# Kernel tuning notes

Measured on AMD Instinct MI355X. Metric: run time of the kernel, lower is better.

The kernel has to match this reference:

```python
import jax, jax.numpy as jnp
import numpy as np

N_NODES = 50000
N_EDGES = 800000
D_FEAT = 64
D_EMB = 64
N_GRAPHS = 512
D_TARGET = 10


def setup_inputs() -> dict:
    key = jax.random.key(0)
    ks = jax.random.split(key, 32)
    x = jax.random.normal(ks[0], (N_NODES, D_FEAT), dtype=jnp.float32)
    edge_index = jax.random.randint(ks[1], (2, N_EDGES), 0, N_NODES, dtype=jnp.int64)
    batch = jnp.sort(jax.random.randint(ks[2], (N_NODES,), 0, N_GRAPHS, dtype=jnp.int64))

    def lin(k, fan_in, fan_out):
        return jax.random.normal(k, (fan_in, fan_out), dtype=jnp.float32) / np.sqrt(fan_in)

    inp = {"x": x, "edge_index": edge_index, "batch": batch}
    # 3 SAGEConv layers: lin_l (neighbors, with bias) + lin_r (root, no bias)
    for i in range(3):
        din = D_FEAT if i == 0 else D_EMB
        inp[f"Wl{i}"] = lin(ks[3 + 3 * i], din, D_EMB)
        inp[f"bl{i}"] = jnp.zeros((D_EMB,), dtype=jnp.float32)
        inp[f"Wr{i}"] = lin(ks[4 + 3 * i], din, D_EMB)
    inp["Wm"] = lin(ks[20], D_EMB, D_EMB)
    inp["bm"] = jnp.zeros((D_EMB,), dtype=jnp.float32)
    inp["W1"] = lin(ks[21], 3 * D_EMB, D_EMB)
    inp["b1"] = jnp.zeros((D_EMB,), dtype=jnp.float32)
    inp["W2"] = lin(ks[22], D_EMB, D_TARGET)
    inp["b2"] = jnp.zeros((D_TARGET,), dtype=jnp.float32)
    return inp


def sage_conv(x, src, dst, Wl, bl, Wr):
    # mean-aggregate neighbor features (messages flow src -> dst)
    agg = jax.ops.segment_sum(x[src], dst, num_segments=N_NODES)
    deg = jax.ops.segment_sum(jnp.ones((src.shape[0],), x.dtype), dst, num_segments=N_NODES)
    mean = agg / jnp.maximum(deg, 1.0)[:, None]
    return mean @ Wl + bl + x @ Wr


def reference(x, edge_index, batch, Wl0, bl0, Wr0, Wl1, bl1, Wr1, Wl2, bl2, Wr2,
              Wm, bm, W1, b1, W2, b2):
    src, dst = edge_index[0], edge_index[1]
    convs = [(Wl0, bl0, Wr0), (Wl1, bl1, Wr1), (Wl2, bl2, Wr2)]
    h = x
    h_all = []
    for Wl, bl, Wr in convs:
        h = sage_conv(h, src, dst, Wl, bl, Wr)
        h = jax.nn.relu(h @ Wm + bm)
        h_all.append(h)
    h = jnp.concatenate(h_all, axis=1)  # [N, 3*D_EMB]
    # global mean pool over graphs
    gsum = jax.ops.segment_sum(h, batch, num_segments=N_GRAPHS)
    gcnt = jax.ops.segment_sum(jnp.ones((h.shape[0],), h.dtype), batch, num_segments=N_GRAPHS)
    g = gsum / jnp.maximum(gcnt, 1.0)[:, None]
    g = jax.nn.relu(g @ W1 + b1)
    return g @ W2 + b2
```

## Files before the change

kernel.cpp:

```cpp
#include <hip/hip_runtime.h>

#define N_NODES 50000
#define N_EDGES 800000
#define D 64
#define N_GRAPHS 512
#define D_TARGET 10
#define NB_SCAN ((N_NODES + 255) / 256)
#define TPAD 72
#define EDGE_BLOCKS (N_EDGES / 256)
#define XSPLIT_BLOCKS EDGE_BLOCKS
#define WPREP_BLOCKS 112

typedef __attribute__((ext_vector_type(8))) short short8;
typedef __attribute__((ext_vector_type(4))) float f32x4;
typedef unsigned short ushort_t;
#define MFMA16(a, b, c) __builtin_amdgcn_mfma_f32_16x16x32_bf16(a, b, c, 0, 0, 0)

__device__ inline unsigned short bf16rne(float f) {
    unsigned u = __builtin_bit_cast(unsigned, f);
    u += 0x7FFFu + ((u >> 16) & 1u);
    return (unsigned short)(u >> 16);
}
__device__ inline float bf2f(unsigned short h) {
    unsigned u = ((unsigned)h) << 16;
    return __builtin_bit_cast(float, u);
}
__device__ inline void acc8(float* a, uint4 v) {
    a[0] += __builtin_bit_cast(float, v.x << 16);
    a[1] += __builtin_bit_cast(float, v.x & 0xFFFF0000u);
    a[2] += __builtin_bit_cast(float, v.y << 16);
    a[3] += __builtin_bit_cast(float, v.y & 0xFFFF0000u);
    a[4] += __builtin_bit_cast(float, v.z << 16);
    a[5] += __builtin_bit_cast(float, v.z & 0xFFFF0000u);
    a[6] += __builtin_bit_cast(float, v.w << 16);
    a[7] += __builtin_bit_cast(float, v.w & 0xFFFF0000u);
}

__global__ void zero_kernel(int* __restrict__ degi) {
    int i = blockIdx.x * 256 + threadIdx.x;
    if (i < N_NODES) degi[i] = 0;
}

__global__ void k1_kernel(const int* __restrict__ dst, const int* __restrict__ batch,
                          int* __restrict__ degi, int* __restrict__ rank,
                          int* __restrict__ gstart,
                          const float* __restrict__ x, ushort_t* __restrict__ xh,
                          const float* __restrict__ w0, const float* __restrict__ w1,
                          const float* __restrict__ w2, const float* __restrict__ w3,
                          const float* __restrict__ w4, const float* __restrict__ w5,
                          const float* __restrict__ w6, short* __restrict__ wfrag) {
    int b = blockIdx.x;
    if (b < EDGE_BLOCKS) {
        int e = b * 256 + threadIdx.x;
        rank[e] = atomicAdd(&degi[dst[e]], 1);
    } else if (b < EDGE_BLOCKS + NB_SCAN) {
        int i = (b - EDGE_BLOCKS) * 256 + threadIdx.x;
        if (i >= N_NODES) return;
        int bb = batch[i];
        int prev = (i == 0) ? -1 : batch[i - 1];
        for (int g = prev + 1; g <= bb; ++g) gstart[g] = i;
        if (i == N_NODES - 1)
            for (int g = bb + 1; g <= N_GRAPHS; ++g) gstart[g] = N_NODES;
    } else if (b < EDGE_BLOCKS + NB_SCAN + XSPLIT_BLOCKS) {
        int idx = (b - EDGE_BLOCKS - NB_SCAN) * 256 + threadIdx.x;
        float4 v = ((const float4*)x)[idx];
        ushort4 o;
        o.x = bf16rne(v.x); o.y = bf16rne(v.y); o.z = bf16rne(v.z); o.w = bf16rne(v.w);
        ((ushort4*)xh)[idx] = o;
    } else {
        int tid = (b - EDGE_BLOCKS - NB_SCAN - XSPLIT_BLOCKS) * 256 + threadIdx.x;
        int m = tid >> 12, t = tid & 4095;
        const float* W = (m == 0) ? w0 : (m == 1) ? w1 : (m == 2) ? w2 : (m == 3) ? w3
                       : (m == 4) ? w4 : (m == 5) ? w5 : w6;
        int j = t & 7, lane = (t >> 3) & 63, nt = (t >> 9) & 3, kt = t >> 11;
        int k = kt * 32 + ((lane >> 4) << 3) + j;
        int o = nt * 16 + (lane & 15);
        float v = W[k * 64 + o];
        unsigned short hi = bf16rne(v);
        unsigned short lo = bf16rne(v - bf2f(hi));
        wfrag[m * 8192 + t]        = (short)hi;
        wfrag[m * 8192 + 4096 + t] = (short)lo;
    }
}

__global__ void scan_partials(const int* __restrict__ degi, int* __restrict__ partial) {
    __shared__ int s[256];
    int t = threadIdx.x;
    int i = blockIdx.x * 256 + t;
    s[t] = (i < N_NODES) ? degi[i] : 0;
    __syncthreads();
    for (int off = 128; off > 0; off >>= 1) {
        if (t < off) s[t] += s[t + off];
        __syncthreads();
    }
    if (t == 0) partial[blockIdx.x] = s[0];
}

__global__ void scan_final(const int* __restrict__ degi, const int* __restrict__ partial,
                           int* __restrict__ rowptr) {
    __shared__ int s[256];
    __shared__ int sp[256];
    int t = threadIdx.x;
    int i = blockIdx.x * 256 + t;
    sp[t] = (t < blockIdx.x) ? partial[t] : 0;
    __syncthreads();
    for (int off = 128; off > 0; off >>= 1) {
        if (t < off) sp[t] += sp[t + off];
        __syncthreads();
    }
    int prefix = sp[0];
    int v = (i < N_NODES) ? degi[i] : 0;
    s[t] = v;
    __syncthreads();
    for (int off = 1; off < 256; off <<= 1) {
        int add = (t >= off) ? s[t - off] : 0;
        __syncthreads();
        s[t] += add;
        __syncthreads();
    }
    if (i < N_NODES) rowptr[i] = prefix + s[t] - v;
    if (i == 0) rowptr[N_NODES] = N_EDGES;
}

__global__ void k4_kernel(const int* __restrict__ src, const int* __restrict__ dst,
                          const int* __restrict__ rank, const int* __restrict__ rowptr,
                          ushort_t* __restrict__ col) {
    int e = blockIdx.x * 256 + threadIdx.x;
    int d = dst[e];
    col[rowptr[d] + rank[e]] = (ushort_t)src[e];
}

__global__ __launch_bounds__(512) void gather_kernel(
    const ushort_t* __restrict__ hplane, const int* __restrict__ rowptr,
    const ushort_t* __restrict__ col,
    ushort_t* __restrict__ mh, ushort_t* __restrict__ ml) {
    int gw   = (blockIdx.x * 512 + threadIdx.x) >> 6;
    int lane = threadIdx.x & 63;
    int f = lane & 7;
    int g = lane >> 3;
    if (gw >= N_NODES) return;
    int beg = rowptr[gw], end = rowptr[gw + 1];
    const uint4* h16 = (const uint4*)hplane;

    float a[8] = {0.f, 0.f, 0.f, 0.f, 0.f, 0.f, 0.f, 0.f};
    float b[8] = {0.f, 0.f, 0.f, 0.f, 0.f, 0.f, 0.f, 0.f};
    int p = beg + g;
    for (; p + 8 < end; p += 16) {
        int s0 = col[p], s1 = col[p + 8];
        uint4 v0 = h16[s0 * 8 + f];
        uint4 v1 = h16[s1 * 8 + f];
        acc8(a, v0);
        acc8(b, v1);
    }
    if (p < end) {
        uint4 v = h16[col[p] * 8 + f];
        acc8(a, v);
    }
#pragma unroll
    for (int j = 0; j < 8; ++j) {
        float v = a[j] + b[j];
        v += __shfl_xor(v, 8);
        v += __shfl_xor(v, 16);
        v += __shfl_xor(v, 32);
        a[j] = v;
    }
    if (g == 0) {
        float inv = 1.0f / fmaxf((float)(end - beg), 1.0f);
        unsigned hws[4], lws[4];
#pragma unroll
        for (int i = 0; i < 4; ++i) {
            float v0 = a[2 * i] * inv, v1 = a[2 * i + 1] * inv;
            unsigned short h0 = bf16rne(v0), h1 = bf16rne(v1);
            hws[i] = (unsigned)h0 | ((unsigned)h1 << 16);
            lws[i] = (unsigned)bf16rne(v0 - bf2f(h0)) |
                     ((unsigned)bf16rne(v1 - bf2f(h1)) << 16);
        }
        uint4 hv = {hws[0], hws[1], hws[2], hws[3]};
        uint4 lv = {lws[0], lws[1], lws[2], lws[3]};
        ((uint4*)mh)[gw * 8 + f] = hv;
        ((uint4*)ml)[gw * 8 + f] = lv;
    }
}

template <int XMODE>
__global__ __launch_bounds__(64) void mm_kernel(
    const float* __restrict__ xf, const ushort_t* __restrict__ xhp,
    const ushort_t* __restrict__ mh, const ushort_t* __restrict__ ml,
    const short* __restrict__ wl, const short* __restrict__ wr, const short* __restrict__ wm,
    const float* __restrict__ blv, const float* __restrict__ bmv,
    ushort_t* __restrict__ hhout) {
    __shared__ short smh[16 * TPAD];
    __shared__ short sml[16 * TPAD];
    __shared__ short sxh[16 * TPAD];
    __shared__ short sxl[16 * TPAD];
    __shared__ short sth[16 * TPAD];
    __shared__ short stl[16 * TPAD];

    int lane = threadIdx.x;
    int f = lane & 15;
    int g = lane >> 4;
    int base = blockIdx.x * 16;

    {
        const uint4* mh16 = (const uint4*)mh;
        const uint4* ml16 = (const uint4*)ml;
#pragma unroll
        for (int i = 0; i < 2; ++i) {
            int c = i * 64 + lane;
            int r = c >> 3, cc = c & 7;
            *(uint4*)&smh[r * TPAD + cc * 8] = mh16[(base + r) * 8 + cc];
            *(uint4*)&sml[r * TPAD + cc * 8] = ml16[(base + r) * 8 + cc];
        }
    }
    if (XMODE == 1) {
        const uint4* xh16 = (const uint4*)xhp;
#pragma unroll
        for (int i = 0; i < 2; ++i) {
            int c = i * 64 + lane;
            int r = c >> 3, cc = c & 7;
            *(uint4*)&sxh[r * TPAD + cc * 8] = xh16[(base + r) * 8 + cc];
        }
    } else {
        const float4* x4 = (const float4*)xf;
#pragma unroll
        for (int i = 0; i < 4; ++i) {
            int idx = i * 64 + lane;
            int r = idx >> 4, c = idx & 15;
            float4 xv = x4[(size_t)(base + r) * 16 + c];
            unsigned short h0 = bf16rne(xv.x), h1 = bf16rne(xv.y),
                           h2 = bf16rne(xv.z), h3 = bf16rne(xv.w);
            uint2 hw, lw;
            hw.x = (unsigned)h0 | ((unsigned)h1 << 16);
            hw.y = (unsigned)h2 | ((unsigned)h3 << 16);
            lw.x = (unsigned)bf16rne(xv.x - bf2f(h0)) | ((unsigned)bf16rne(xv.y - bf2f(h1)) << 16);
            lw.y = (unsigned)bf16rne(xv.z - bf2f(h2)) | ((unsigned)bf16rne(xv.w - bf2f(h3)) << 16);
            *(uint2*)&sxh[r * TPAD + c * 4] = hw;
            *(uint2*)&sxl[r * TPAD + c * 4] = lw;
        }
    }

    short8 amh[2], aml[2], axh[2], axl[2];
#pragma unroll
    for (int kt = 0; kt < 2; ++kt) {
        int idx = f * TPAD + kt * 32 + g * 8;
        amh[kt] = *(const short8*)&smh[idx];
        aml[kt] = *(const short8*)&sml[idx];
        axh[kt] = *(const short8*)&sxh[idx];
        if (XMODE == 0) axl[kt] = *(const short8*)&sxl[idx];
    }
    const short* wlh = wl;
    const short* wll = wl + 4096;
    const short* wrh = wr;
    const short* wrl = wr + 4096;

#pragma unroll
    for (int nt = 0; nt < 4; ++nt) {
        f32x4 acc = {0.f, 0.f, 0.f, 0.f};
#pragma unroll
        for (int kt = 0; kt < 2; ++kt) {
            int fi = ((kt * 4 + nt) * 64 + lane) * 8;
            short8 blh = *(const short8*)&wlh[fi];
            short8 bll = *(const short8*)&wll[fi];
            short8 brh = *(const short8*)&wrh[fi];
            short8 brl = *(const short8*)&wrl[fi];
            acc = MFMA16(amh[kt], blh, acc);
            acc = MFMA16(aml[kt], blh, acc);
            acc = MFMA16(amh[kt], bll, acc);
            acc = MFMA16(axh[kt], brh, acc);
            if (XMODE == 0) acc = MFMA16(axl[kt], brh, acc);
            acc = MFMA16(axh[kt], brl, acc);
        }
        float bias = blv[nt * 16 + f];
#pragma unroll
        for (int r = 0; r < 4; ++r) {
            float tv = acc[r] + bias;
            unsigned short hi = bf16rne(tv);
            unsigned short lo = bf16rne(tv - bf2f(hi));
            int row = g * 4 + r;
            sth[row * TPAD + nt * 16 + f] = (short)hi;
            stl[row * TPAD + nt * 16 + f] = (short)lo;
        }
    }

    short8 ath[2], atl[2];
#pragma unroll
    for (int kt = 0; kt < 2; ++kt) {
        int idx = f * TPAD + kt * 32 + g * 8;
        ath[kt] = *(const short8*)&sth[idx];
        atl[kt] = *(const short8*)&stl[idx];
    }
    const short* wmh = wm;
    const short* wml = wm + 4096;
#pragma unroll
    for (int nt = 0; nt < 4; ++nt) {
        f32x4 acc = {0.f, 0.f, 0.f, 0.f};
#pragma unroll
        for (int kt = 0; kt < 2; ++kt) {
            int fi = ((kt * 4 + nt) * 64 + lane) * 8;
            short8 bh  = *(const short8*)&wmh[fi];
            short8 bl2 = *(const short8*)&wml[fi];
            acc = MFMA16(ath[kt], bh, acc);
            acc = MFMA16(atl[kt], bh, acc);
            acc = MFMA16(ath[kt], bl2, acc);
        }
        float bias = bmv[nt * 16 + f];
#pragma unroll
        for (int r = 0; r < 4; ++r) {
            float hv = acc[r] + bias;
            hv = hv > 0.f ? hv : 0.f;
            int row  = g * 4 + r;
            int node = base + row;
            hhout[node * D + nt * 16 + f] = bf16rne(hv);
        }
    }
}

__global__ __launch_bounds__(256) void poolmlp_kernel(
    const ushort_t* __restrict__ h0, const ushort_t* __restrict__ h1,
    const ushort_t* __restrict__ h2, const int* __restrict__ gstart,
    const float* __restrict__ W1, const float* __restrict__ b1,
    const float* __restrict__ W2, const float* __restrict__ b2,
    float* __restrict__ out) {
    __shared__ float spart[4][3][64];
    __shared__ float sg[3 * 64];
    __shared__ float tt[64];
    int gr = blockIdx.x;
    int w = threadIdx.x >> 6, lane = threadIdx.x & 63;
    int beg = gstart[gr], end = gstart[gr + 1];
    float s0 = 0.f, s1 = 0.f, s2 = 0.f;
    for (int n = beg + w; n < end; n += 4) {
        s0 += bf2f(h0[n * 64 + lane]);
        s1 += bf2f(h1[n * 64 + lane]);
        s2 += bf2f(h2[n * 64 + lane]);
    }
    spart[w][0][lane] = s0; spart[w][1][lane] = s1; spart[w][2][lane] = s2;
    __syncthreads();
    if (w == 0) {
        float inv = 1.0f / fmaxf((float)(end - beg), 1.0f);
#pragma unroll
        for (int l = 0; l < 3; ++l)
            sg[l * 64 + lane] = (spart[0][l][lane] + spart[1][l][lane] +
                                 spart[2][l][lane] + spart[3][l][lane]) * inv;
    }
    __syncthreads();
    if (w == 0) {
        float acc = b1[lane];
#pragma unroll 8
        for (int k = 0; k < 3 * 64; ++k) acc += sg[k] * W1[k * 64 + lane];
        tt[lane] = fmaxf(acc, 0.f);
    }
    __syncthreads();
    if (w == 0 && lane < D_TARGET) {
        float acc = b2[lane];
#pragma unroll
        for (int k = 0; k < 64; ++k) acc += tt[k] * W2[k * D_TARGET + lane];
        out[gr * D_TARGET + lane] = acc;
    }
}

extern "C" void kernel_launch(void* const* d_in, const int* in_sizes, int n_in,
                              void* d_out, int out_size, void* d_ws, size_t ws_size,
                              hipStream_t stream) {
    const float* x     = (const float*)d_in[0];
    const int*   ei    = (const int*)d_in[1];
    const int*   src   = ei;
    const int*   dst   = ei + N_EDGES;
    const int*   batch = (const int*)d_in[2];

    const float* Wl[3] = {(const float*)d_in[3], (const float*)d_in[6], (const float*)d_in[9]};
    const float* bl[3] = {(const float*)d_in[4], (const float*)d_in[7], (const float*)d_in[10]};
    const float* Wr[3] = {(const float*)d_in[5], (const float*)d_in[8], (const float*)d_in[11]};
    const float* Wm = (const float*)d_in[12];
    const float* bm = (const float*)d_in[13];
    const float* W1 = (const float*)d_in[14];
    const float* b1 = (const float*)d_in[15];
    const float* W2 = (const float*)d_in[16];
    const float* b2 = (const float*)d_in[17];

    int*      degi    = (int*)d_ws;
    int*      partial = degi + 50000;
    int*      rowptr  = partial + 256;
    int*      rank    = rowptr + 50008;
    int*      gstart  = rank + 800000;
    short*    wfrag   = (short*)(gstart + 520);
    ushort_t* col     = (ushort_t*)(wfrag + 7 * 8192);
    ushort_t* xh      = col + 800000;
    ushort_t* mh      = xh + (size_t)N_NODES * D;
    ushort_t* ml      = mh + (size_t)N_NODES * D;
    ushort_t* hh0     = ml + (size_t)N_NODES * D;
    ushort_t* hh1     = hh0 + (size_t)N_NODES * D;
    ushort_t* hh2     = hh1 + (size_t)N_NODES * D;

    zero_kernel<<<NB_SCAN, 256, 0, stream>>>(degi);

    k1_kernel<<<EDGE_BLOCKS + NB_SCAN + XSPLIT_BLOCKS + WPREP_BLOCKS, 256, 0, stream>>>(
        dst, batch, degi, rank, gstart, x, xh,
        Wl[0], Wr[0], Wl[1], Wr[1], Wl[2], Wr[2], Wm, wfrag);
    scan_partials<<<NB_SCAN, 256, 0, stream>>>(degi, partial);
    scan_final<<<NB_SCAN, 256, 0, stream>>>(degi, partial, rowptr);
    k4_kernel<<<EDGE_BLOCKS, 256, 0, stream>>>(src, dst, rank, rowptr, col);

    ushort_t* hplanes[4] = {xh, hh0, hh1, hh2};
    for (int l = 0; l < 3; ++l) {
        gather_kernel<<<(N_NODES * 64 + 511) / 512, 512, 0, stream>>>(
            hplanes[l], rowptr, col, mh, ml);
        if (l == 0)
            mm_kernel<0><<<N_NODES / 16, 64, 0, stream>>>(
                x, nullptr, mh, ml,
                wfrag + 0 * 8192, wfrag + 1 * 8192, wfrag + 6 * 8192,
                bl[0], bm, hh0);
        else
            mm_kernel<1><<<N_NODES / 16, 64, 0, stream>>>(
                nullptr, hplanes[l], mh, ml,
                wfrag + (2 * l) * 8192, wfrag + (2 * l + 1) * 8192, wfrag + 6 * 8192,
                bl[l], bm, hplanes[l + 1]);
    }

    poolmlp_kernel<<<N_GRAPHS, 256, 0, stream>>>(hh0, hh1, hh2, gstart, W1, b1, W2, b2,
                                                 (float*)d_out);
}
```

Before: 185.9 us.

## Split degree-count atomics across eight partitioned counter arrays

The per-destination degree counting in the CSR build now uses eight separate counter arrays, chosen by block index, so that contended atomics on the same node are spread out. A new combine kernel turns the per-partition counts into exclusive offsets and totals per node, and the column-scatter kernel adds the partition offset to each edge's local rank. The cost is an extra kernel launch, eight times more counters to zero and read, and an extra gather of the offset in the scatter step. Edge order within a node's row changes, so the floating-point sum order in the gather differs slightly.

After: 186.8 us. No clear change (+0.5%).

```diff
diff --git a/kernel.cpp b/kernel.cpp
--- a/kernel.cpp
+++ b/kernel.cpp
@@ -10,6 +10,8 @@
 #define EDGE_BLOCKS (N_EDGES / 256)
 #define XSPLIT_BLOCKS EDGE_BLOCKS
 #define WPREP_BLOCKS 112
+#define NPART 8
+#define PSTRIDE 50048
 
 typedef __attribute__((ext_vector_type(8))) short short8;
 typedef __attribute__((ext_vector_type(4))) float f32x4;
@@ -36,13 +38,13 @@
     a[7] += __builtin_bit_cast(float, v.w & 0xFFFF0000u);
 }
 
-__global__ void zero_kernel(int* __restrict__ degi) {
+__global__ void zero_kernel(int* __restrict__ deg8) {
     int i = blockIdx.x * 256 + threadIdx.x;
-    if (i < N_NODES) degi[i] = 0;
+    if (i < NPART * PSTRIDE) deg8[i] = 0;
 }
 
 __global__ void k1_kernel(const int* __restrict__ dst, const int* __restrict__ batch,
-                          int* __restrict__ degi, int* __restrict__ rank,
+                          int* __restrict__ deg8, int* __restrict__ rank,
                           int* __restrict__ gstart,
                           const float* __restrict__ x, ushort_t* __restrict__ xh,
                           const float* __restrict__ w0, const float* __restrict__ w1,
@@ -51,8 +53,10 @@
                           const float* __restrict__ w6, short* __restrict__ wfrag) {
     int b = blockIdx.x;
     if (b < EDGE_BLOCKS) {
+        int part = b & (NPART - 1);
         int e = b * 256 + threadIdx.x;
-        rank[e] = atomicAdd(&degi[dst[e]], 1);
+        int lr = atomicAdd(&deg8[part * PSTRIDE + dst[e]], 1);
+        rank[e] = (part << 24) | lr;
     } else if (b < EDGE_BLOCKS + NB_SCAN) {
         int i = (b - EDGE_BLOCKS) * 256 + threadIdx.x;
         if (i >= N_NODES) return;
@@ -83,6 +87,19 @@
     }
 }
 
+__global__ void combine_kernel(int* __restrict__ deg8, int* __restrict__ degi) {
+    int i = blockIdx.x * 256 + threadIdx.x;
+    if (i >= N_NODES) return;
+    int run = 0;
+#pragma unroll
+    for (int p = 0; p < NPART; ++p) {
+        int c = deg8[p * PSTRIDE + i];
+        deg8[p * PSTRIDE + i] = run;
+        run += c;
+    }
+    degi[i] = run;
+}
+
 __global__ void scan_partials(const int* __restrict__ degi, int* __restrict__ partial) {
     __shared__ int s[256];
     int t = threadIdx.x;
@@ -124,10 +141,13 @@
 
 __global__ void k4_kernel(const int* __restrict__ src, const int* __restrict__ dst,
                           const int* __restrict__ rank, const int* __restrict__ rowptr,
-                          ushort_t* __restrict__ col) {
+                          const int* __restrict__ deg8, ushort_t* __restrict__ col) {
     int e = blockIdx.x * 256 + threadIdx.x;
     int d = dst[e];
-    col[rowptr[d] + rank[e]] = (ushort_t)src[e];
+    int r = rank[e];
+    int part = r >> 24;
+    int pos = rowptr[d] + deg8[part * PSTRIDE + d] + (r & 0xFFFFFF);
+    col[pos] = (ushort_t)src[e];
 }
 
 __global__ __launch_bounds__(512) void gather_kernel(
@@ -377,7 +397,8 @@
     const float* W2 = (const float*)d_in[16];
     const float* b2 = (const float*)d_in[17];
 
-    int*      degi    = (int*)d_ws;
+    int*      deg8    = (int*)d_ws;
+    int*      degi    = deg8 + NPART * PSTRIDE;
     int*      partial = degi + 50000;
     int*      rowptr  = partial + 256;
     int*      rank    = rowptr + 50008;
@@ -391,14 +412,15 @@
     ushort_t* hh1     = hh0 + (size_t)N_NODES * D;
     ushort_t* hh2     = hh1 + (size_t)N_NODES * D;
 
-    zero_kernel<<<NB_SCAN, 256, 0, stream>>>(degi);
+    zero_kernel<<<(NPART * PSTRIDE + 255) / 256, 256, 0, stream>>>(deg8);
 
     k1_kernel<<<EDGE_BLOCKS + NB_SCAN + XSPLIT_BLOCKS + WPREP_BLOCKS, 256, 0, stream>>>(
-        dst, batch, degi, rank, gstart, x, xh,
+        dst, batch, deg8, rank, gstart, x, xh,
         Wl[0], Wr[0], Wl[1], Wr[1], Wl[2], Wr[2], Wm, wfrag);
+    combine_kernel<<<NB_SCAN, 256, 0, stream>>>(deg8, degi);
     scan_partials<<<NB_SCAN, 256, 0, stream>>>(degi, partial);
     scan_final<<<NB_SCAN, 256, 0, stream>>>(degi, partial, rowptr);
-    k4_kernel<<<EDGE_BLOCKS, 256, 0, stream>>>(src, dst, rank, rowptr, col);
+    k4_kernel<<<EDGE_BLOCKS, 256, 0, stream>>>(src, dst, rank, rowptr, deg8, col);
 
     ushort_t* hplanes[4] = {xh, hh0, hh1, hh2};
     for (int l = 0; l < 3; ++l) {
```

## Fuse neighbor gather with SAGE matmuls into one kernel per layer

Applied to the files above, without the earlier changes.

Merges the mean-aggregation gather kernel and the MFMA matmul kernel into a single 1024-thread block per 16 nodes. Each of the 16 waves gathers one node's neighbors into shared memory, then four waves run the Wl/Wr and Wm MFMA stages. This removes the global round-trip of the split-bf16 mean planes and half the kernel launches. In exchange, 12 of 16 waves sit idle during the matmul phase, and the large blocks may limit occupancy and tail behaviour.

Result: slower. 202.1 us (+8.7%).

```diff
diff --git a/kernel.cpp b/kernel.cpp
--- a/kernel.cpp
+++ b/kernel.cpp
@@ -130,62 +130,10 @@
     col[rowptr[d] + rank[e]] = (ushort_t)src[e];
 }
 
-__global__ __launch_bounds__(512) void gather_kernel(
-    const ushort_t* __restrict__ hplane, const int* __restrict__ rowptr,
-    const ushort_t* __restrict__ col,
-    ushort_t* __restrict__ mh, ushort_t* __restrict__ ml) {
-    int gw   = (blockIdx.x * 512 + threadIdx.x) >> 6;
-    int lane = threadIdx.x & 63;
-    int f = lane & 7;
-    int g = lane >> 3;
-    if (gw >= N_NODES) return;
-    int beg = rowptr[gw], end = rowptr[gw + 1];
-    const uint4* h16 = (const uint4*)hplane;
-
-    float a[8] = {0.f, 0.f, 0.f, 0.f, 0.f, 0.f, 0.f, 0.f};
-    float b[8] = {0.f, 0.f, 0.f, 0.f, 0.f, 0.f, 0.f, 0.f};
-    int p = beg + g;
-    for (; p + 8 < end; p += 16) {
-        int s0 = col[p], s1 = col[p + 8];
-        uint4 v0 = h16[s0 * 8 + f];
-        uint4 v1 = h16[s1 * 8 + f];
-        acc8(a, v0);
-        acc8(b, v1);
-    }
-    if (p < end) {
-        uint4 v = h16[col[p] * 8 + f];
-        acc8(a, v);
-    }
-#pragma unroll
-    for (int j = 0; j < 8; ++j) {
-        float v = a[j] + b[j];
-        v += __shfl_xor(v, 8);
-        v += __shfl_xor(v, 16);
-        v += __shfl_xor(v, 32);
-        a[j] = v;
-    }
-    if (g == 0) {
-        float inv = 1.0f / fmaxf((float)(end - beg), 1.0f);
-        unsigned hws[4], lws[4];
-#pragma unroll
-        for (int i = 0; i < 4; ++i) {
-            float v0 = a[2 * i] * inv, v1 = a[2 * i + 1] * inv;
-            unsigned short h0 = bf16rne(v0), h1 = bf16rne(v1);
-            hws[i] = (unsigned)h0 | ((unsigned)h1 << 16);
-            lws[i] = (unsigned)bf16rne(v0 - bf2f(h0)) |
-                     ((unsigned)bf16rne(v1 - bf2f(h1)) << 16);
-        }
-        uint4 hv = {hws[0], hws[1], hws[2], hws[3]};
-        uint4 lv = {lws[0], lws[1], lws[2], lws[3]};
-        ((uint4*)mh)[gw * 8 + f] = hv;
-        ((uint4*)ml)[gw * 8 + f] = lv;
-    }
-}
-
 template <int XMODE>
-__global__ __launch_bounds__(64) void mm_kernel(
-    const float* __restrict__ xf, const ushort_t* __restrict__ xhp,
-    const ushort_t* __restrict__ mh, const ushort_t* __restrict__ ml,
+__global__ __launch_bounds__(1024) void sage_fused(
+    const float* __restrict__ xf, const ushort_t* __restrict__ hplane,
+    const int* __restrict__ rowptr, const ushort_t* __restrict__ col,
     const short* __restrict__ wl, const short* __restrict__ wr, const short* __restrict__ wm,
     const float* __restrict__ blv, const float* __restrict__ bmv,
     ushort_t* __restrict__ hhout) {
@@ -196,65 +144,99 @@
     __shared__ short sth[16 * TPAD];
     __shared__ short stl[16 * TPAD];
 
-    int lane = threadIdx.x;
+    int tid  = threadIdx.x;
+    int wid  = tid >> 6;
+    int lane = tid & 63;
+    int f8 = lane & 7;
+    int g8 = lane >> 3;
+    int base = blockIdx.x * 16;
+    int node = base + wid;
+    const uint4* h16 = (const uint4*)hplane;
+
+    {
+        int beg = rowptr[node], end = rowptr[node + 1];
+        float a[8] = {0.f, 0.f, 0.f, 0.f, 0.f, 0.f, 0.f, 0.f};
+        float b[8] = {0.f, 0.f, 0.f, 0.f, 0.f, 0.f, 0.f, 0.f};
+        int p = beg + g8;
+        for (; p + 8 < end; p += 16) {
+            int s0 = col[p], s1 = col[p + 8];
+            uint4 v0 = h16[s0 * 8 + f8];
+            uint4 v1 = h16[s1 * 8 + f8];
+            acc8(a, v0);
+            acc8(b, v1);
+        }
+        if (p < end) {
+            uint4 v = h16[col[p] * 8 + f8];
+            acc8(a, v);
+        }
+#pragma unroll
+        for (int j = 0; j < 8; ++j) {
+            float v = a[j] + b[j];
+            v += __shfl_xor(v, 8);
+            v += __shfl_xor(v, 16);
+            v += __shfl_xor(v, 32);
+            a[j] = v;
+        }
+        if (g8 == 0) {
+            float inv = 1.0f / fmaxf((float)(end - beg), 1.0f);
+            unsigned hws[4], lws[4];
+#pragma unroll
+            for (int i = 0; i < 4; ++i) {
+                float v0 = a[2 * i] * inv, v1 = a[2 * i + 1] * inv;
+                unsigned short h0 = bf16rne(v0), h1 = bf16rne(v1);
+                hws[i] = (unsigned)h0 | ((unsigned)h1 << 16);
+                lws[i] = (unsigned)bf16rne(v0 - bf2f(h0)) |
+                         ((unsigned)bf16rne(v1 - bf2f(h1)) << 16);
+            }
+            uint4 hv = {hws[0], hws[1], hws[2], hws[3]};
+            uint4 lv = {lws[0], lws[1], lws[2], lws[3]};
+            *(uint4*)&smh[wid * TPAD + f8 * 8] = hv;
+            *(uint4*)&sml[wid * TPAD + f8 * 8] = lv;
+        } else if (g8 == 1) {
+            if (XMODE == 1) {
+                uint4 v = h16[node * 8 + f8];
+                *(uint4*)&sxh[wid * TPAD + f8 * 8] = v;
+            } else {
+                const float4* x4 = (const float4*)xf;
+                float4 v0 = x4[(size_t)node * 16 + f8 * 2];
+                float4 v1 = x4[(size_t)node * 16 + f8 * 2 + 1];
+                unsigned short h0 = bf16rne(v0.x), h1 = bf16rne(v0.y),
+                               h2 = bf16rne(v0.z), h3 = bf16rne(v0.w);
+                unsigned short h4 = bf16rne(v1.x), h5 = bf16rne(v1.y),
+                               h6 = bf16rne(v1.z), h7 = bf16rne(v1.w);
+                uint4 hv, lv;
+                hv.x = (unsigned)h0 | ((unsigned)h1 << 16);
+                hv.y = (unsigned)h2 | ((unsigned)h3 << 16);
+                hv.z = (unsigned)h4 | ((unsigned)h5 << 16);
+                hv.w = (unsigned)h6 | ((unsigned)h7 << 16);
+                lv.x = (unsigned)bf16rne(v0.x - bf2f(h0)) | ((unsigned)bf16rne(v0.y - bf2f(h1)) << 16);
+                lv.y = (unsigned)bf16rne(v0.z - bf2f(h2)) | ((unsigned)bf16rne(v0.w - bf2f(h3)) << 16);
+                lv.z = (unsigned)bf16rne(v1.x - bf2f(h4)) | ((unsigned)bf16rne(v1.y - bf2f(h5)) << 16);
+                lv.w = (unsigned)bf16rne(v1.z - bf2f(h6)) | ((unsigned)bf16rne(v1.w - bf2f(h7)) << 16);
+                *(uint4*)&sxh[wid * TPAD + f8 * 8] = hv;
+                *(uint4*)&sxl[wid * TPAD + f8 * 8] = lv;
+            }
+        }
+    }
+    __syncthreads();
+
     int f = lane & 15;
     int g = lane >> 4;
-    int base = blockIdx.x * 16;
-
-    {
-        const uint4* mh16 = (const uint4*)mh;
-        const uint4* ml16 = (const uint4*)ml;
-#pragma unroll
-        for (int i = 0; i < 2; ++i) {
-            int c = i * 64 + lane;
-            int r = c >> 3, cc = c & 7;
-            *(uint4*)&smh[r * TPAD + cc * 8] = mh16[(base + r) * 8 + cc];
-            *(uint4*)&sml[r * TPAD + cc * 8] = ml16[(base + r) * 8 + cc];
-        }
-    }
-    if (XMODE == 1) {
-        const uint4* xh16 = (const uint4*)xhp;
-#pragma unroll
-        for (int i = 0; i < 2; ++i) {
-            int c = i * 64 + lane;
-            int r = c >> 3, cc = c & 7;
-            *(uint4*)&sxh[r * TPAD + cc * 8] = xh16[(base + r) * 8 + cc];
-        }
-    } else {
-        const float4* x4 = (const float4*)xf;
-#pragma unroll
-        for (int i = 0; i < 4; ++i) {
-            int idx = i * 64 + lane;
-            int r = idx >> 4, c = idx & 15;
-            float4 xv = x4[(size_t)(base + r) * 16 + c];
-            unsigned short h0 = bf16rne(xv.x), h1 = bf16rne(xv.y),
-                           h2 = bf16rne(xv.z), h3 = bf16rne(xv.w);
-            uint2 hw, lw;
-            hw.x = (unsigned)h0 | ((unsigned)h1 << 16);
-            hw.y = (unsigned)h2 | ((unsigned)h3 << 16);
-            lw.x = (unsigned)bf16rne(xv.x - bf2f(h0)) | ((unsigned)bf16rne(xv.y - bf2f(h1)) << 16);
-            lw.y = (unsigned)bf16rne(xv.z - bf2f(h2)) | ((unsigned)bf16rne(xv.w - bf2f(h3)) << 16);
-            *(uint2*)&sxh[r * TPAD + c * 4] = hw;
-            *(uint2*)&sxl[r * TPAD + c * 4] = lw;
-        }
-    }
-
-    short8 amh[2], aml[2], axh[2], axl[2];
-#pragma unroll
-    for (int kt = 0; kt < 2; ++kt) {
-        int idx = f * TPAD + kt * 32 + g * 8;
-        amh[kt] = *(const short8*)&smh[idx];
-        aml[kt] = *(const short8*)&sml[idx];
-        axh[kt] = *(const short8*)&sxh[idx];
-        if (XMODE == 0) axl[kt] = *(const short8*)&sxl[idx];
-    }
-    const short* wlh = wl;
-    const short* wll = wl + 4096;
-    const short* wrh = wr;
-    const short* wrl = wr + 4096;
-
-#pragma unroll
-    for (int nt = 0; nt < 4; ++nt) {
+    if (wid < 4) {
+        int nt = wid;
+        short8 amh[2], aml[2], axh[2], axl[2];
+#pragma unroll
+        for (int kt = 0; kt < 2; ++kt) {
+            int idx = f * TPAD + kt * 32 + g * 8;
+            amh[kt] = *(const short8*)&smh[idx];
+            aml[kt] = *(const short8*)&sml[idx];
+            axh[kt] = *(const short8*)&sxh[idx];
+            if (XMODE == 0) axl[kt] = *(const short8*)&sxl[idx];
+        }
+        const short* wlh = wl;
+        const short* wll = wl + 4096;
+        const short* wrh = wr;
+        const short* wrl = wr + 4096;
         f32x4 acc = {0.f, 0.f, 0.f, 0.f};
 #pragma unroll
         for (int kt = 0; kt < 2; ++kt) {
@@ -281,18 +263,19 @@
             stl[row * TPAD + nt * 16 + f] = (short)lo;
         }
     }
-
-    short8 ath[2], atl[2];
-#pragma unroll
-    for (int kt = 0; kt < 2; ++kt) {
-        int idx = f * TPAD + kt * 32 + g * 8;
-        ath[kt] = *(const short8*)&sth[idx];
-        atl[kt] = *(const short8*)&stl[idx];
-    }
-    const short* wmh = wm;
-    const short* wml = wm + 4096;
-#pragma unroll
-    for (int nt = 0; nt < 4; ++nt) {
+    __syncthreads();
+
+    if (wid < 4) {
+        int nt = wid;
+        short8 ath[2], atl[2];
+#pragma unroll
+        for (int kt = 0; kt < 2; ++kt) {
+            int idx = f * TPAD + kt * 32 + g * 8;
+            ath[kt] = *(const short8*)&sth[idx];
+            atl[kt] = *(const short8*)&stl[idx];
+        }
+        const short* wmh = wm;
+        const short* wml = wm + 4096;
         f32x4 acc = {0.f, 0.f, 0.f, 0.f};
 #pragma unroll
         for (int kt = 0; kt < 2; ++kt) {
@@ -309,8 +292,8 @@
             float hv = acc[r] + bias;
             hv = hv > 0.f ? hv : 0.f;
             int row  = g * 4 + r;
-            int node = base + row;
-            hhout[node * D + nt * 16 + f] = bf16rne(hv);
+            int onode = base + row;
+            hhout[onode * D + nt * 16 + f] = bf16rne(hv);
         }
     }
 }
@@ -385,9 +368,7 @@
     short*    wfrag   = (short*)(gstart + 520);
     ushort_t* col     = (ushort_t*)(wfrag + 7 * 8192);
     ushort_t* xh      = col + 800000;
-    ushort_t* mh      = xh + (size_t)N_NODES * D;
-    ushort_t* ml      = mh + (size_t)N_NODES * D;
-    ushort_t* hh0     = ml + (size_t)N_NODES * D;
+    ushort_t* hh0     = xh + (size_t)N_NODES * D;
     ushort_t* hh1     = hh0 + (size_t)N_NODES * D;
     ushort_t* hh2     = hh1 + (size_t)N_NODES * D;
 
@@ -400,21 +381,15 @@
     scan_final<<<NB_SCAN, 256, 0, stream>>>(degi, partial, rowptr);
     k4_kernel<<<EDGE_BLOCKS, 256, 0, stream>>>(src, dst, rank, rowptr, col);
 
-    ushort_t* hplanes[4] = {xh, hh0, hh1, hh2};
-    for (int l = 0; l < 3; ++l) {
-        gather_kernel<<<(N_NODES * 64 + 511) / 512, 512, 0, stream>>>(
-            hplanes[l], rowptr, col, mh, ml);
-        if (l == 0)
-            mm_kernel<0><<<N_NODES / 16, 64, 0, stream>>>(
-                x, nullptr, mh, ml,
-                wfrag + 0 * 8192, wfrag + 1 * 8192, wfrag + 6 * 8192,
-                bl[0], bm, hh0);
-        else
-            mm_kernel<1><<<N_NODES / 16, 64, 0, stream>>>(
-                nullptr, hplanes[l], mh, ml,
-                wfrag + (2 * l) * 8192, wfrag + (2 * l + 1) * 8192, wfrag + 6 * 8192,
-                bl[l], bm, hplanes[l + 1]);
-    }
+    sage_fused<0><<<N_NODES / 16, 1024, 0, stream>>>(
+        x, xh, rowptr, col,
+        wfrag + 0 * 8192, wfrag + 1 * 8192, wfrag + 6 * 8192, bl[0], bm, hh0);
+    sage_fused<1><<<N_NODES / 16, 1024, 0, stream>>>(
+        nullptr, hh0, rowptr, col,
+        wfrag + 2 * 8192, wfrag + 3 * 8192, wfrag + 6 * 8192, bl[1], bm, hh1);
+    sage_fused<1><<<N_NODES / 16, 1024, 0, stream>>>(
+        nullptr, hh1, rowptr, col,
+        wfrag + 4 * 8192, wfrag + 5 * 8192, wfrag + 6 * 8192, bl[2], bm, hh2);
 
     poolmlp_kernel<<<N_GRAPHS, 256, 0, stream>>>(hh0, hh1, hh2, gstart, W1, b1, W2, b2,
                                                  (float*)d_out);
```
